# Kernel optimization log

Measured on AMD Instinct MI355X. Metric: run time of the kernel, lower is better.

The kernel has to match this reference:

```python
import jax, jax.numpy as jnp
import numpy as np

N_NODES = 100000
N_EDGES = 1600000
N_FEAT = 100
HIDDEN = 64
N_CLASSES = 47


def setup_inputs() -> dict:
    key = jax.random.key(0)
    k1, k2, k3, k4 = jax.random.split(key, 4)
    x = jax.random.normal(k1, (N_NODES, N_FEAT), dtype=jnp.float32)
    edge_index = jax.random.randint(k2, (2, N_EDGES), 0, N_NODES, dtype=jnp.int64)
    # Glorot-style init for GCNConv weights; zero bias (PyG default)
    W0 = jax.random.normal(k3, (N_FEAT, HIDDEN), dtype=jnp.float32) * (1.0 / np.sqrt(N_FEAT))
    b0 = jnp.zeros((HIDDEN,), dtype=jnp.float32)
    W1 = jax.random.normal(k4, (HIDDEN, N_CLASSES), dtype=jnp.float32) * (1.0 / np.sqrt(HIDDEN))
    b1 = jnp.zeros((N_CLASSES,), dtype=jnp.float32)
    return {"x": x, "edge_index": edge_index, "W0": W0, "b0": b0, "W1": W1, "b1": b1}


def _gcn_norm(edge_index, n_nodes):
    # PyG gcn_norm with add_self_loops=True, edge_weight=1
    loop = jnp.arange(n_nodes, dtype=edge_index.dtype)
    row = jnp.concatenate([edge_index[0], loop])  # source nodes
    col = jnp.concatenate([edge_index[1], loop])  # destination nodes
    ones = jnp.ones(row.shape[0], dtype=jnp.float32)
    deg = jax.ops.segment_sum(ones, col, num_segments=n_nodes)
    dinv = jnp.where(deg > 0, jax.lax.rsqrt(deg), 0.0)
    norm = dinv[row] * dinv[col]  # [E + N]
    return row, col, norm


def _gcn_conv(x, W, b, row, col, norm, n_nodes):
    # GCNConv: transform, then gather-scale-scatter aggregate, then bias
    xw = x @ W                                   # [N, out]
    msg = norm[:, None] * xw[row]                # [E+N, out]
    out = jax.ops.segment_sum(msg, col, num_segments=n_nodes)
    return out + b


def reference(x, edge_index, W0, b0, W1, b1):
    n_nodes = x.shape[0]
    row, col, norm = _gcn_norm(edge_index, n_nodes)  # same graph -> same norm per layer (cached)
    h = _gcn_conv(x, W0, b0, row, col, norm, n_nodes)
    h = jax.nn.relu(h)  # dropout is identity in eval mode
    out = _gcn_conv(h, W1, b1, row, col, norm, n_nodes)
    return out
```

## Files before the change

kernel.cpp:

```cpp
#include <hip/hip_runtime.h>
#include <hip/hip_fp16.h>

#define N_NODES   100000
#define N_EDGES   1600000
#define N_FEAT    100
#define HIDDEN    64
#define N_CLASSES 47
#define ZPAD      48
#define NBIN      ((N_NODES + 255) / 256)
#define SBLK      256
#define CHUNK     (N_EDGES / SBLK)
#define NHIST     (NBIN * SBLK)
#define WT0_ELEMS (HIDDEN * 128)
#define WT1_ELEMS (ZPAD * 64)

typedef _Float16 f16x8 __attribute__((ext_vector_type(8)));
typedef float f32x4 __attribute__((ext_vector_type(4)));


__global__ __launch_bounds__(256) void k_gscan1(const int* __restrict__ in,
                                                int* __restrict__ out,
                                                int* __restrict__ sums, int n) {
    __shared__ int tmp[256];
    int i = blockIdx.x * 256 + threadIdx.x;
    int v = (i < n) ? in[i] : 0;
    tmp[threadIdx.x] = v;
    __syncthreads();
    for (int off = 1; off < 256; off <<= 1) {
        int t = (threadIdx.x >= off) ? tmp[threadIdx.x - off] : 0;
        __syncthreads();
        tmp[threadIdx.x] += t;
        __syncthreads();
    }
    if (i < n) out[i] = tmp[threadIdx.x] - v;
    if (threadIdx.x == 255) sums[blockIdx.x] = tmp[255];
}

__global__ __launch_bounds__(512) void k_gscan2(int* __restrict__ sums, int nb) {
    __shared__ int tmp[512];
    int i = threadIdx.x;
    int v = (i < nb) ? sums[i] : 0;
    tmp[i] = v;
    __syncthreads();
    for (int off = 1; off < 512; off <<= 1) {
        int t = (i >= off) ? tmp[i - off] : 0;
        __syncthreads();
        tmp[i] += t;
        __syncthreads();
    }
    if (i < nb) sums[i] = tmp[i] - v;
}


__global__ __launch_bounds__(256) void k_hist(const int* __restrict__ ecol,
                                              int* __restrict__ gh) {
    __shared__ int lh[NBIN];
    int b = blockIdx.x, t = threadIdx.x;
    for (int i = t; i < NBIN; i += 256) lh[i] = 0;
    __syncthreads();
    int e0 = b * CHUNK;
    for (int i = t; i < CHUNK; i += 256)
        atomicAdd(&lh[ecol[e0 + i] >> 8], 1);
    __syncthreads();
    for (int i = t; i < NBIN; i += 256) gh[i * SBLK + b] = lh[i];
}

__global__ __launch_bounds__(256) void k_radix_scatter(
    const int* __restrict__ erow, const int* __restrict__ ecol,
    const int* __restrict__ gpos, const int* __restrict__ hsums,
    int* __restrict__ pairs) {
    __shared__ int lc[NBIN];
    int b = blockIdx.x, t = threadIdx.x;
    for (int i = t; i < NBIN; i += 256) lc[i] = gpos[i * SBLK + b] + hsums[i];
    __syncthreads();
    int e0 = b * CHUNK;
    for (int i = t; i < CHUNK; i += 256) {
        int e = e0 + i;
        int r = erow[e], c = ecol[e];
        int pos = atomicAdd(&lc[c >> 8], 1);
        pairs[pos] = r | ((c & 255) << 17);
    }
}

__global__ __launch_bounds__(256) void k_binfinish(
    const int* __restrict__ gpos, const int* __restrict__ hsums,
    const int* __restrict__ pairs,
    int* __restrict__ rp, float* __restrict__ dinv, int* __restrict__ eidx) {
    __shared__ int cnt[256];
    __shared__ int tmp[256];
    int b = blockIdx.x, t = threadIdx.x;
    int n0 = b << 8;
    int beg = gpos[b * SBLK] + hsums[b];
    int end = (b + 1 < NBIN) ? gpos[(b + 1) * SBLK] + hsums[b + 1] : N_EDGES;

    cnt[t] = 0;
    __syncthreads();
    for (int i = beg + t; i < end; i += 256)
        atomicAdd(&cnt[(pairs[i] >> 17) & 255], 1);
    __syncthreads();
    int v = cnt[t];
    tmp[t] = v;
    __syncthreads();
    for (int off = 1; off < 256; off <<= 1) {
        int u = (t >= off) ? tmp[t - off] : 0;
        __syncthreads();
        tmp[t] += u;
        __syncthreads();
    }
    int rpv = beg + tmp[t] - v;
    int n = n0 + t;
    if (n < N_NODES) {
        rp[n] = rpv;
        dinv[n] = rsqrtf(1.0f + (float)v);
    }
    if (b == NBIN - 1 && t == 0) rp[N_NODES] = N_EDGES;
    cnt[t] = rpv;
    __syncthreads();
    for (int i = beg + t; i < end; i += 256) {
        int p = pairs[i];
        int pos = atomicAdd(&cnt[(p >> 17) & 255], 1);
        eidx[pos] = p & 0x1FFFF;
    }
}

__global__ __launch_bounds__(256) void k_wprep(const float* __restrict__ W0,
                                               const float* __restrict__ W1,
                                               __half* __restrict__ wt0,
                                               __half* __restrict__ wt1) {
    int i = blockIdx.x * 256 + threadIdx.x;
    if (i < WT0_ELEMS) {
        int n = i >> 7, k = i & 127;
        wt0[i] = __float2half((k < N_FEAT) ? W0[k * HIDDEN + n] : 0.0f);
    } else if (i < WT0_ELEMS + WT1_ELEMS) {
        int j = i - WT0_ELEMS;
        int n = j >> 6, k = j & 63;
        wt1[j] = __float2half((n < N_CLASSES) ? W1[k * N_CLASSES + n] : 0.0f);
    }
}

__global__ __launch_bounds__(256) void k_gemm1(
    const float* __restrict__ x, const __half* __restrict__ wt0,
    const float* __restrict__ dinv, __half* __restrict__ yh) {
    int w = threadIdx.x >> 6, l = threadIdx.x & 63;
    int g = l >> 4, c16 = l & 15;
    int row = blockIdx.x * 64 + w * 16 + c16;
    int rl = (row < N_NODES) ? row : (N_NODES - 1);
    const float* xr = x + (size_t)rl * N_FEAT;

    f16x8 a[4];
    #pragma unroll
    for (int s = 0; s < 4; ++s) {
        int k0 = 32 * s + 8 * g;
        float4 f0 = (k0 + 3 < N_FEAT) ? *(const float4*)(xr + k0)
                                      : make_float4(0.f, 0.f, 0.f, 0.f);
        float4 f1 = (k0 + 7 < N_FEAT) ? *(const float4*)(xr + k0 + 4)
                                      : make_float4(0.f, 0.f, 0.f, 0.f);
        a[s][0] = (_Float16)f0.x; a[s][1] = (_Float16)f0.y;
        a[s][2] = (_Float16)f0.z; a[s][3] = (_Float16)f0.w;
        a[s][4] = (_Float16)f1.x; a[s][5] = (_Float16)f1.y;
        a[s][6] = (_Float16)f1.z; a[s][7] = (_Float16)f1.w;
    }
    f32x4 acc0 = {0,0,0,0}, acc1 = {0,0,0,0}, acc2 = {0,0,0,0}, acc3 = {0,0,0,0};
    #pragma unroll
    for (int s = 0; s < 4; ++s) {
        int ko = 32 * s + 8 * g;
        f16x8 b0 = *(const f16x8*)(wt0 + (0 * 16 + c16) * 128 + ko);
        f16x8 b1 = *(const f16x8*)(wt0 + (1 * 16 + c16) * 128 + ko);
        f16x8 b2 = *(const f16x8*)(wt0 + (2 * 16 + c16) * 128 + ko);
        f16x8 b3 = *(const f16x8*)(wt0 + (3 * 16 + c16) * 128 + ko);
        acc0 = __builtin_amdgcn_mfma_f32_16x16x32_f16(a[s], b0, acc0, 0, 0, 0);
        acc1 = __builtin_amdgcn_mfma_f32_16x16x32_f16(a[s], b1, acc1, 0, 0, 0);
        acc2 = __builtin_amdgcn_mfma_f32_16x16x32_f16(a[s], b2, acc2, 0, 0, 0);
        acc3 = __builtin_amdgcn_mfma_f32_16x16x32_f16(a[s], b3, acc3, 0, 0, 0);
    }
    int orow = blockIdx.x * 64 + w * 16 + 4 * g;
    #pragma unroll
    for (int r = 0; r < 4; ++r) {
        if (orow + r < N_NODES) {
            float di = dinv[orow + r];
            size_t base = (size_t)(orow + r) * HIDDEN + c16;
            yh[base +  0] = __float2half(di * acc0[r]);
            yh[base + 16] = __float2half(di * acc1[r]);
            yh[base + 32] = __float2half(di * acc2[r]);
            yh[base + 48] = __float2half(di * acc3[r]);
        }
    }
}

__global__ __launch_bounds__(256) void k_agg0(
    const int* __restrict__ rp, const int* __restrict__ eidx,
    const float* __restrict__ dinv, const __half* __restrict__ yh,
    const float* __restrict__ b0, const __half* __restrict__ wt1,
    __half* __restrict__ zh) {
    __shared__ __half hs[16][64];
    int t = blockIdx.x * 256 + threadIdx.x;
    int n = t >> 5;
    int hl = threadIdx.x & 31;
    int nl = threadIdx.x >> 5;

    ((__half2*)hs)[256 + threadIdx.x] = __floats2half2_rn(0.f, 0.f);

    int beg = rp[n], end = rp[n + 1];
    int deg = end - beg;
    int se = (beg + hl < end) ? eidx[beg + hl] : 0;
    const __half2* yh2 = (const __half2*)yh;
    float2 fs = __half22float2(yh2[(size_t)n * 32 + hl]);
    float ax = fs.x, ay = fs.y;
    int m = deg < 32 ? deg : 32;
    int base = threadIdx.x & 32;

    {
        int s0 = __shfl(se, base + 0),  s1 = __shfl(se, base + 1);
        int s2 = __shfl(se, base + 2),  s3 = __shfl(se, base + 3);
        int s4 = __shfl(se, base + 4),  s5 = __shfl(se, base + 5);
        int s6 = __shfl(se, base + 6),  s7 = __shfl(se, base + 7);
        int s8 = __shfl(se, base + 8),  s9 = __shfl(se, base + 9);
        int sa = __shfl(se, base + 10), sb = __shfl(se, base + 11);
        int sc = __shfl(se, base + 12), sd = __shfl(se, base + 13);
        int sec = __shfl(se, base + 14), sf = __shfl(se, base + 15);
        float2 f0 = __half22float2(yh2[(size_t)s0 * 32 + hl]);
        float2 f1 = __half22float2(yh2[(size_t)s1 * 32 + hl]);
        float2 f2 = __half22float2(yh2[(size_t)s2 * 32 + hl]);
        float2 f3 = __half22float2(yh2[(size_t)s3 * 32 + hl]);
        float2 f4 = __half22float2(yh2[(size_t)s4 * 32 + hl]);
        float2 f5 = __half22float2(yh2[(size_t)s5 * 32 + hl]);
        float2 f6 = __half22float2(yh2[(size_t)s6 * 32 + hl]);
        float2 f7 = __half22float2(yh2[(size_t)s7 * 32 + hl]);
        float2 f8 = __half22float2(yh2[(size_t)s8 * 32 + hl]);
        float2 f9 = __half22float2(yh2[(size_t)s9 * 32 + hl]);
        float2 fa = __half22float2(yh2[(size_t)sa * 32 + hl]);
        float2 fb = __half22float2(yh2[(size_t)sb * 32 + hl]);
        float2 fc = __half22float2(yh2[(size_t)sc * 32 + hl]);
        float2 fd = __half22float2(yh2[(size_t)sd * 32 + hl]);
        float2 fe = __half22float2(yh2[(size_t)sec * 32 + hl]);
        float2 ff = __half22float2(yh2[(size_t)sf * 32 + hl]);
        ax += ((m > 0  ? f0.x : 0.f) + (m > 1  ? f1.x : 0.f)) +
              ((m > 2  ? f2.x : 0.f) + (m > 3  ? f3.x : 0.f)) +
              ((m > 4  ? f4.x : 0.f) + (m > 5  ? f5.x : 0.f)) +
              ((m > 6  ? f6.x : 0.f) + (m > 7  ? f7.x : 0.f)) +
              ((m > 8  ? f8.x : 0.f) + (m > 9  ? f9.x : 0.f)) +
              ((m > 10 ? fa.x : 0.f) + (m > 11 ? fb.x : 0.f)) +
              ((m > 12 ? fc.x : 0.f) + (m > 13 ? fd.x : 0.f)) +
              ((m > 14 ? fe.x : 0.f) + (m > 15 ? ff.x : 0.f));
        ay += ((m > 0  ? f0.y : 0.f) + (m > 1  ? f1.y : 0.f)) +
              ((m > 2  ? f2.y : 0.f) + (m > 3  ? f3.y : 0.f)) +
              ((m > 4  ? f4.y : 0.f) + (m > 5  ? f5.y : 0.f)) +
              ((m > 6  ? f6.y : 0.f) + (m > 7  ? f7.y : 0.f)) +
              ((m > 8  ? f8.y : 0.f) + (m > 9  ? f9.y : 0.f)) +
              ((m > 10 ? fa.y : 0.f) + (m > 11 ? fb.y : 0.f)) +
              ((m > 12 ? fc.y : 0.f) + (m > 13 ? fd.y : 0.f)) +
              ((m > 14 ? fe.y : 0.f) + (m > 15 ? ff.y : 0.f));
    }
    if (m > 16) {
        int s0 = __shfl(se, base + 16), s1 = __shfl(se, base + 17);
        int s2 = __shfl(se, base + 18), s3 = __shfl(se, base + 19);
        int s4 = __shfl(se, base + 20), s5 = __shfl(se, base + 21);
        int s6 = __shfl(se, base + 22), s7 = __shfl(se, base + 23);
        int s8 = __shfl(se, base + 24), s9 = __shfl(se, base + 25);
        int sa = __shfl(se, base + 26), sb = __shfl(se, base + 27);
        int sc = __shfl(se, base + 28), sd = __shfl(se, base + 29);
        int sec = __shfl(se, base + 30), sf = __shfl(se, base + 31);
        float2 f0 = __half22float2(yh2[(size_t)s0 * 32 + hl]);
        float2 f1 = __half22float2(yh2[(size_t)s1 * 32 + hl]);
        float2 f2 = __half22float2(yh2[(size_t)s2 * 32 + hl]);
        float2 f3 = __half22float2(yh2[(size_t)s3 * 32 + hl]);
        float2 f4 = __half22float2(yh2[(size_t)s4 * 32 + hl]);
        float2 f5 = __half22float2(yh2[(size_t)s5 * 32 + hl]);
        float2 f6 = __half22float2(yh2[(size_t)s6 * 32 + hl]);
        float2 f7 = __half22float2(yh2[(size_t)s7 * 32 + hl]);
        float2 f8 = __half22float2(yh2[(size_t)s8 * 32 + hl]);
        float2 f9 = __half22float2(yh2[(size_t)s9 * 32 + hl]);
        float2 fa = __half22float2(yh2[(size_t)sa * 32 + hl]);
        float2 fb = __half22float2(yh2[(size_t)sb * 32 + hl]);
        float2 fc = __half22float2(yh2[(size_t)sc * 32 + hl]);
        float2 fd = __half22float2(yh2[(size_t)sd * 32 + hl]);
        float2 fe = __half22float2(yh2[(size_t)sec * 32 + hl]);
        float2 ff = __half22float2(yh2[(size_t)sf * 32 + hl]);
        ax += ((m > 16 ? f0.x : 0.f) + (m > 17 ? f1.x : 0.f)) +
              ((m > 18 ? f2.x : 0.f) + (m > 19 ? f3.x : 0.f)) +
              ((m > 20 ? f4.x : 0.f) + (m > 21 ? f5.x : 0.f)) +
              ((m > 22 ? f6.x : 0.f) + (m > 23 ? f7.x : 0.f)) +
              ((m > 24 ? f8.x : 0.f) + (m > 25 ? f9.x : 0.f)) +
              ((m > 26 ? fa.x : 0.f) + (m > 27 ? fb.x : 0.f)) +
              ((m > 28 ? fc.x : 0.f) + (m > 29 ? fd.x : 0.f)) +
              ((m > 30 ? fe.x : 0.f) + (m > 31 ? ff.x : 0.f));
        ay += ((m > 16 ? f0.y : 0.f) + (m > 17 ? f1.y : 0.f)) +
              ((m > 18 ? f2.y : 0.f) + (m > 19 ? f3.y : 0.f)) +
              ((m > 20 ? f4.y : 0.f) + (m > 21 ? f5.y : 0.f)) +
              ((m > 22 ? f6.y : 0.f) + (m > 23 ? f7.y : 0.f)) +
              ((m > 24 ? f8.y : 0.f) + (m > 25 ? f9.y : 0.f)) +
              ((m > 26 ? fa.y : 0.f) + (m > 27 ? fb.y : 0.f)) +
              ((m > 28 ? fc.y : 0.f) + (m > 29 ? fd.y : 0.f)) +
              ((m > 30 ? fe.y : 0.f) + (m > 31 ? ff.y : 0.f));
    }
    if (deg > 32) {
        for (int e = beg + 32; e < end; ++e) {
            int s = eidx[e];
            float2 fv = __half22float2(yh2[(size_t)s * 32 + hl]);
            ax += fv.x; ay += fv.y;
        }
    }
    float di = dinv[n];
    float2 b2 = ((const float2*)b0)[hl];
    float o0 = fmaxf(di * ax + b2.x, 0.0f);
    float o1 = fmaxf(di * ay + b2.y, 0.0f);
    ((__half2*)hs)[nl * 32 + hl] = __floats2half2_rn(o0, o1);
    __syncthreads();

    if (threadIdx.x < 64) {
        int l = threadIdx.x;
        int g = l >> 4, c16 = l & 15;
        f16x8 a0 = *(const f16x8*)(&hs[c16][8 * g]);
        f16x8 a1 = *(const f16x8*)(&hs[c16][32 + 8 * g]);
        f32x4 acc0 = {0,0,0,0}, acc1 = {0,0,0,0}, acc2 = {0,0,0,0};
        #pragma unroll
        for (int s = 0; s < 2; ++s) {
            int ko = 32 * s + 8 * g;
            f16x8 b0f = *(const f16x8*)(wt1 + (0 * 16 + c16) * 64 + ko);
            f16x8 b1f = *(const f16x8*)(wt1 + (1 * 16 + c16) * 64 + ko);
            f16x8 b2f = *(const f16x8*)(wt1 + (2 * 16 + c16) * 64 + ko);
            f16x8 av = s ? a1 : a0;
            acc0 = __builtin_amdgcn_mfma_f32_16x16x32_f16(av, b0f, acc0, 0, 0, 0);
            acc1 = __builtin_amdgcn_mfma_f32_16x16x32_f16(av, b1f, acc1, 0, 0, 0);
            acc2 = __builtin_amdgcn_mfma_f32_16x16x32_f16(av, b2f, acc2, 0, 0, 0);
        }
        if (g < 2) {
            int nrow = blockIdx.x * 8 + 4 * g;
            #pragma unroll
            for (int r = 0; r < 4; ++r) {
                float dr = dinv[nrow + r];
                size_t bz = (size_t)(nrow + r) * ZPAD + c16;
                zh[bz +  0] = __float2half(dr * acc0[r]);
                zh[bz + 16] = __float2half(dr * acc1[r]);
                zh[bz + 32] = __float2half(dr * acc2[r]);
            }
        }
    }
}

__global__ __launch_bounds__(256) void k_agg1(
    const int* __restrict__ rp, const int* __restrict__ eidx,
    const float* __restrict__ dinv, const __half* __restrict__ zh,
    const float* __restrict__ b1, float* __restrict__ out) {
    int t = blockIdx.x * 256 + threadIdx.x;
    int n = t >> 5;
    int hl = threadIdx.x & 31;
    if (n >= N_NODES) return;
    int beg = rp[n], end = rp[n + 1];
    int deg = end - beg;
    int se = (beg + hl < end) ? eidx[beg + hl] : 0;
    const __half2* zh2 = (const __half2*)zh;
    float ax = 0.0f, ay = 0.0f;
    if (hl < 24) {
        float2 f = __half22float2(zh2[(size_t)n * 24 + hl]);
        ax = f.x; ay = f.y;
    }
    int m = deg < 32 ? deg : 32;
    int base = threadIdx.x & 32;

    {
        int s0 = __shfl(se, base + 0),  s1 = __shfl(se, base + 1);
        int s2 = __shfl(se, base + 2),  s3 = __shfl(se, base + 3);
        int s4 = __shfl(se, base + 4),  s5 = __shfl(se, base + 5);
        int s6 = __shfl(se, base + 6),  s7 = __shfl(se, base + 7);
        int s8 = __shfl(se, base + 8),  s9 = __shfl(se, base + 9);
        int sa = __shfl(se, base + 10), sb = __shfl(se, base + 11);
        int sc = __shfl(se, base + 12), sd = __shfl(se, base + 13);
        int sec = __shfl(se, base + 14), sf = __shfl(se, base + 15);
        if (hl < 24) {
            float2 f0 = __half22float2(zh2[(size_t)s0 * 24 + hl]);
            float2 f1 = __half22float2(zh2[(size_t)s1 * 24 + hl]);
            float2 f2 = __half22float2(zh2[(size_t)s2 * 24 + hl]);
            float2 f3 = __half22float2(zh2[(size_t)s3 * 24 + hl]);
            float2 f4 = __half22float2(zh2[(size_t)s4 * 24 + hl]);
            float2 f5 = __half22float2(zh2[(size_t)s5 * 24 + hl]);
            float2 f6 = __half22float2(zh2[(size_t)s6 * 24 + hl]);
            float2 f7 = __half22float2(zh2[(size_t)s7 * 24 + hl]);
            float2 f8 = __half22float2(zh2[(size_t)s8 * 24 + hl]);
            float2 f9 = __half22float2(zh2[(size_t)s9 * 24 + hl]);
            float2 fa = __half22float2(zh2[(size_t)sa * 24 + hl]);
            float2 fb = __half22float2(zh2[(size_t)sb * 24 + hl]);
            float2 fc = __half22float2(zh2[(size_t)sc * 24 + hl]);
            float2 fd = __half22float2(zh2[(size_t)sd * 24 + hl]);
            float2 fe = __half22float2(zh2[(size_t)sec * 24 + hl]);
            float2 ff = __half22float2(zh2[(size_t)sf * 24 + hl]);
            ax += ((m > 0  ? f0.x : 0.f) + (m > 1  ? f1.x : 0.f)) +
                  ((m > 2  ? f2.x : 0.f) + (m > 3  ? f3.x : 0.f)) +
                  ((m > 4  ? f4.x : 0.f) + (m > 5  ? f5.x : 0.f)) +
                  ((m > 6  ? f6.x : 0.f) + (m > 7  ? f7.x : 0.f)) +
                  ((m > 8  ? f8.x : 0.f) + (m > 9  ? f9.x : 0.f)) +
                  ((m > 10 ? fa.x : 0.f) + (m > 11 ? fb.x : 0.f)) +
                  ((m > 12 ? fc.x : 0.f) + (m > 13 ? fd.x : 0.f)) +
                  ((m > 14 ? fe.x : 0.f) + (m > 15 ? ff.x : 0.f));
            ay += ((m > 0  ? f0.y : 0.f) + (m > 1  ? f1.y : 0.f)) +
                  ((m > 2  ? f2.y : 0.f) + (m > 3  ? f3.y : 0.f)) +
                  ((m > 4  ? f4.y : 0.f) + (m > 5  ? f5.y : 0.f)) +
                  ((m > 6  ? f6.y : 0.f) + (m > 7  ? f7.y : 0.f)) +
                  ((m > 8  ? f8.y : 0.f) + (m > 9  ? f9.y : 0.f)) +
                  ((m > 10 ? fa.y : 0.f) + (m > 11 ? fb.y : 0.f)) +
                  ((m > 12 ? fc.y : 0.f) + (m > 13 ? fd.y : 0.f)) +
                  ((m > 14 ? fe.y : 0.f) + (m > 15 ? ff.y : 0.f));
        }
    }
    if (m > 16) {
        int s0 = __shfl(se, base + 16), s1 = __shfl(se, base + 17);
        int s2 = __shfl(se, base + 18), s3 = __shfl(se, base + 19);
        int s4 = __shfl(se, base + 20), s5 = __shfl(se, base + 21);
        int s6 = __shfl(se, base + 22), s7 = __shfl(se, base + 23);
        int s8 = __shfl(se, base + 24), s9 = __shfl(se, base + 25);
        int sa = __shfl(se, base + 26), sb = __shfl(se, base + 27);
        int sc = __shfl(se, base + 28), sd = __shfl(se, base + 29);
        int sec = __shfl(se, base + 30), sf = __shfl(se, base + 31);
        if (hl < 24) {
            float2 f0 = __half22float2(zh2[(size_t)s0 * 24 + hl]);
            float2 f1 = __half22float2(zh2[(size_t)s1 * 24 + hl]);
            float2 f2 = __half22float2(zh2[(size_t)s2 * 24 + hl]);
            float2 f3 = __half22float2(zh2[(size_t)s3 * 24 + hl]);
            float2 f4 = __half22float2(zh2[(size_t)s4 * 24 + hl]);
            float2 f5 = __half22float2(zh2[(size_t)s5 * 24 + hl]);
            float2 f6 = __half22float2(zh2[(size_t)s6 * 24 + hl]);
            float2 f7 = __half22float2(zh2[(size_t)s7 * 24 + hl]);
            float2 f8 = __half22float2(zh2[(size_t)s8 * 24 + hl]);
            float2 f9 = __half22float2(zh2[(size_t)s9 * 24 + hl]);
            float2 fa = __half22float2(zh2[(size_t)sa * 24 + hl]);
            float2 fb = __half22float2(zh2[(size_t)sb * 24 + hl]);
            float2 fc = __half22float2(zh2[(size_t)sc * 24 + hl]);
            float2 fd = __half22float2(zh2[(size_t)sd * 24 + hl]);
            float2 fe = __half22float2(zh2[(size_t)sec * 24 + hl]);
            float2 ff = __half22float2(zh2[(size_t)sf * 24 + hl]);
            ax += ((m > 16 ? f0.x : 0.f) + (m > 17 ? f1.x : 0.f)) +
                  ((m > 18 ? f2.x : 0.f) + (m > 19 ? f3.x : 0.f)) +
                  ((m > 20 ? f4.x : 0.f) + (m > 21 ? f5.x : 0.f)) +
                  ((m > 22 ? f6.x : 0.f) + (m > 23 ? f7.x : 0.f)) +
                  ((m > 24 ? f8.x : 0.f) + (m > 25 ? f9.x : 0.f)) +
                  ((m > 26 ? fa.x : 0.f) + (m > 27 ? fb.x : 0.f)) +
                  ((m > 28 ? fc.x : 0.f) + (m > 29 ? fd.x : 0.f)) +
                  ((m > 30 ? fe.x : 0.f) + (m > 31 ? ff.x : 0.f));
            ay += ((m > 16 ? f0.y : 0.f) + (m > 17 ? f1.y : 0.f)) +
                  ((m > 18 ? f2.y : 0.f) + (m > 19 ? f3.y : 0.f)) +
                  ((m > 20 ? f4.y : 0.f) + (m > 21 ? f5.y : 0.f)) +
                  ((m > 22 ? f6.y : 0.f) + (m > 23 ? f7.y : 0.f)) +
                  ((m > 24 ? f8.y : 0.f) + (m > 25 ? f9.y : 0.f)) +
                  ((m > 26 ? fa.y : 0.f) + (m > 27 ? fb.y : 0.f)) +
                  ((m > 28 ? fc.y : 0.f) + (m > 29 ? fd.y : 0.f)) +
                  ((m > 30 ? fe.y : 0.f) + (m > 31 ? ff.y : 0.f));
        }
    }
    if (deg > 32) {
        for (int e = beg + 32; e < end; ++e) {
            int s = eidx[e];
            if (hl < 24) {
                float2 fv = __half22float2(zh2[(size_t)s * 24 + hl]);
                ax += fv.x; ay += fv.y;
            }
        }
    }
    if (hl < 24) {
        float di = dinv[n];
        out[(size_t)n * N_CLASSES + 2 * hl] = di * ax + b1[2 * hl];
        if (hl < 23)
            out[(size_t)n * N_CLASSES + 2 * hl + 1] = di * ay + b1[2 * hl + 1];
    }
}

extern "C" void kernel_launch(void* const* d_in, const int* in_sizes, int n_in,
                              void* d_out, int out_size, void* d_ws, size_t ws_size,
                              hipStream_t stream) {
    const float* x  = (const float*)d_in[0];
    const int*   ei = (const int*)d_in[1];
    const float* W0 = (const float*)d_in[2];
    const float* b0 = (const float*)d_in[3];
    const float* W1 = (const float*)d_in[4];
    const float* b1 = (const float*)d_in[5];
    float* out = (float*)d_out;

    char* ws = (char*)d_ws;
    float*  dinv  = (float*)(ws);
    int*    rp    = (int*)(ws + 412 * 1024);
    int*    hsums = (int*)(ws + 824 * 1024);
    int*    gh    = (int*)(ws + 828 * 1024);
    int*    gpos  = (int*)(ws + 1232 * 1024);
    __half* wt0   = (__half*)(ws + 1640 * 1024);
    __half* wt1   = (__half*)(ws + 1660 * 1024);
    int*    eidx  = (int*)(ws + 1668 * 1024);
    __half* yh    = (__half*)(ws + 9ull * 1024 * 1024);
    __half* zh    = (__half*)(ws + 22ull * 1024 * 1024);
    int*    pairs = (int*)zh;

    const int* erow = ei;
    const int* ecol = ei + N_EDGES;

    k_hist  <<<SBLK, 256, 0, stream>>>(ecol, gh);
    k_gscan1<<<NBIN, 256, 0, stream>>>(gh, gpos, hsums, NHIST);
    k_gscan2<<<1, 512, 0, stream>>>(hsums, NBIN);
    k_radix_scatter<<<SBLK, 256, 0, stream>>>(erow, ecol, gpos, hsums, pairs);
    k_binfinish<<<NBIN, 256, 0, stream>>>(gpos, hsums, pairs, rp, dinv, eidx);

    k_wprep<<<(WT0_ELEMS + WT1_ELEMS + 255) / 256, 256, 0, stream>>>(W0, W1, wt0, wt1);

    k_gemm1<<<(N_NODES + 63) / 64, 256, 0, stream>>>(x, wt0, dinv, yh);
    k_agg0 <<<(N_NODES * 32) / 256, 256, 0, stream>>>(rp, eidx, dinv, yh, b0, wt1, zh);

    k_agg1 <<<(N_NODES * 32) / 256, 256, 0, stream>>>(rp, eidx, dinv, zh, b1, out);
}
```

Measured before the change: 137.1 us.

## Fold weight prep into histogram kernel, double sort blocks, widen bin-finish blocks

Removes the separate weight-conversion kernel launch by doing the fp16 weight transpose inside the histogram kernel, whose 512 blocks cover all weight elements. The radix-sort partition count rises from 256 to 512, so each block handles a smaller edge chunk and the scan kernels use 512-thread blocks to match. The bin-finish kernel moves to 1024 threads per block so the counting and placement loops over each bin run with more parallelism. In exchange the global histogram and scan grow larger, and the workspace offsets are shifted to fit them.

```diff
diff --git a/kernel.cpp b/kernel.cpp
--- a/kernel.cpp
+++ b/kernel.cpp
@@ -8,32 +8,33 @@
 #define N_CLASSES 47
 #define ZPAD      48
 #define NBIN      ((N_NODES + 255) / 256)
-#define SBLK      256
+#define SBLK      512
 #define CHUNK     (N_EDGES / SBLK)
 #define NHIST     (NBIN * SBLK)
 #define WT0_ELEMS (HIDDEN * 128)
 #define WT1_ELEMS (ZPAD * 64)
+#define WPREP_N   (WT0_ELEMS + WT1_ELEMS)
 
 typedef _Float16 f16x8 __attribute__((ext_vector_type(8)));
 typedef float f32x4 __attribute__((ext_vector_type(4)));
 
 
-__global__ __launch_bounds__(256) void k_gscan1(const int* __restrict__ in,
+__global__ __launch_bounds__(512) void k_gscan1(const int* __restrict__ in,
                                                 int* __restrict__ out,
                                                 int* __restrict__ sums, int n) {
-    __shared__ int tmp[256];
-    int i = blockIdx.x * 256 + threadIdx.x;
+    __shared__ int tmp[512];
+    int i = blockIdx.x * 512 + threadIdx.x;
     int v = (i < n) ? in[i] : 0;
     tmp[threadIdx.x] = v;
     __syncthreads();
-    for (int off = 1; off < 256; off <<= 1) {
+    for (int off = 1; off < 512; off <<= 1) {
         int t = (threadIdx.x >= off) ? tmp[threadIdx.x - off] : 0;
         __syncthreads();
         tmp[threadIdx.x] += t;
         __syncthreads();
     }
     if (i < n) out[i] = tmp[threadIdx.x] - v;
-    if (threadIdx.x == 255) sums[blockIdx.x] = tmp[255];
+    if (threadIdx.x == 511) sums[blockIdx.x] = tmp[511];
 }
 
 __global__ __launch_bounds__(512) void k_gscan2(int* __restrict__ sums, int nb) {
@@ -53,7 +54,21 @@
 
 
 __global__ __launch_bounds__(256) void k_hist(const int* __restrict__ ecol,
-                                              int* __restrict__ gh) {
+                                              int* __restrict__ gh,
+                                              const float* __restrict__ W0,
+                                              const float* __restrict__ W1,
+                                              __half* __restrict__ wt0,
+                                              __half* __restrict__ wt1) {
+    int wi = blockIdx.x * 256 + threadIdx.x;
+    if (wi < WT0_ELEMS) {
+        int n = wi >> 7, k = wi & 127;
+        wt0[wi] = __float2half((k < N_FEAT) ? W0[k * HIDDEN + n] : 0.0f);
+    } else if (wi < WPREP_N) {
+        int j = wi - WT0_ELEMS;
+        int n = j >> 6, k = j & 63;
+        wt1[j] = __float2half((n < N_CLASSES) ? W1[k * N_CLASSES + n] : 0.0f);
+    }
+
     __shared__ int lh[NBIN];
     int b = blockIdx.x, t = threadIdx.x;
     for (int i = t; i < NBIN; i += 256) lh[i] = 0;
@@ -82,7 +97,7 @@
     }
 }
 
-__global__ __launch_bounds__(256) void k_binfinish(
+__global__ __launch_bounds__(1024) void k_binfinish(
     const int* __restrict__ gpos, const int* __restrict__ hsums,
     const int* __restrict__ pairs,
     int* __restrict__ rp, float* __restrict__ dinv, int* __restrict__ eidx) {
@@ -93,48 +108,35 @@
     int beg = gpos[b * SBLK] + hsums[b];
     int end = (b + 1 < NBIN) ? gpos[(b + 1) * SBLK] + hsums[b + 1] : N_EDGES;
 
-    cnt[t] = 0;
-    __syncthreads();
-    for (int i = beg + t; i < end; i += 256)
+    if (t < 256) cnt[t] = 0;
+    __syncthreads();
+    for (int i = beg + t; i < end; i += 1024)
         atomicAdd(&cnt[(pairs[i] >> 17) & 255], 1);
     __syncthreads();
-    int v = cnt[t];
-    tmp[t] = v;
+    int v = 0;
+    if (t < 256) { v = cnt[t]; tmp[t] = v; }
     __syncthreads();
     for (int off = 1; off < 256; off <<= 1) {
-        int u = (t >= off) ? tmp[t - off] : 0;
+        int u = (t < 256 && t >= off) ? tmp[t - off] : 0;
         __syncthreads();
-        tmp[t] += u;
+        if (t < 256) tmp[t] += u;
         __syncthreads();
     }
-    int rpv = beg + tmp[t] - v;
-    int n = n0 + t;
-    if (n < N_NODES) {
-        rp[n] = rpv;
-        dinv[n] = rsqrtf(1.0f + (float)v);
+    if (t < 256) {
+        int rpv = beg + tmp[t] - v;
+        int n = n0 + t;
+        if (n < N_NODES) {
+            rp[n] = rpv;
+            dinv[n] = rsqrtf(1.0f + (float)v);
+        }
+        cnt[t] = rpv;
     }
     if (b == NBIN - 1 && t == 0) rp[N_NODES] = N_EDGES;
-    cnt[t] = rpv;
-    __syncthreads();
-    for (int i = beg + t; i < end; i += 256) {
+    __syncthreads();
+    for (int i = beg + t; i < end; i += 1024) {
         int p = pairs[i];
         int pos = atomicAdd(&cnt[(p >> 17) & 255], 1);
         eidx[pos] = p & 0x1FFFF;
-    }
-}
-
-__global__ __launch_bounds__(256) void k_wprep(const float* __restrict__ W0,
-                                               const float* __restrict__ W1,
-                                               __half* __restrict__ wt0,
-                                               __half* __restrict__ wt1) {
-    int i = blockIdx.x * 256 + threadIdx.x;
-    if (i < WT0_ELEMS) {
-        int n = i >> 7, k = i & 127;
-        wt0[i] = __float2half((k < N_FEAT) ? W0[k * HIDDEN + n] : 0.0f);
-    } else if (i < WT0_ELEMS + WT1_ELEMS) {
-        int j = i - WT0_ELEMS;
-        int n = j >> 6, k = j & 63;
-        wt1[j] = __float2half((n < N_CLASSES) ? W1[k * N_CLASSES + n] : 0.0f);
     }
 }
 
@@ -479,24 +481,22 @@
     int*    rp    = (int*)(ws + 412 * 1024);
     int*    hsums = (int*)(ws + 824 * 1024);
     int*    gh    = (int*)(ws + 828 * 1024);
-    int*    gpos  = (int*)(ws + 1232 * 1024);
-    __half* wt0   = (__half*)(ws + 1640 * 1024);
-    __half* wt1   = (__half*)(ws + 1660 * 1024);
-    int*    eidx  = (int*)(ws + 1668 * 1024);
-    __half* yh    = (__half*)(ws + 9ull * 1024 * 1024);
-    __half* zh    = (__half*)(ws + 22ull * 1024 * 1024);
+    int*    gpos  = (int*)(ws + 1612 * 1024);
+    __half* wt0   = (__half*)(ws + 2400 * 1024);
+    __half* wt1   = (__half*)(ws + 2420 * 1024);
+    int*    eidx  = (int*)(ws + 2428 * 1024);
+    __half* yh    = (__half*)(ws + 10ull * 1024 * 1024);
+    __half* zh    = (__half*)(ws + 23ull * 1024 * 1024);
     int*    pairs = (int*)zh;
 
     const int* erow = ei;
     const int* ecol = ei + N_EDGES;
 
-    k_hist  <<<SBLK, 256, 0, stream>>>(ecol, gh);
-    k_gscan1<<<NBIN, 256, 0, stream>>>(gh, gpos, hsums, NHIST);
+    k_hist  <<<SBLK, 256, 0, stream>>>(ecol, gh, W0, W1, wt0, wt1);
+    k_gscan1<<<NBIN, 512, 0, stream>>>(gh, gpos, hsums, NHIST);
     k_gscan2<<<1, 512, 0, stream>>>(hsums, NBIN);
     k_radix_scatter<<<SBLK, 256, 0, stream>>>(erow, ecol, gpos, hsums, pairs);
-    k_binfinish<<<NBIN, 256, 0, stream>>>(gpos, hsums, pairs, rp, dinv, eidx);
-
-    k_wprep<<<(WT0_ELEMS + WT1_ELEMS + 255) / 256, 256, 0, stream>>>(W0, W1, wt0, wt1);
+    k_binfinish<<<NBIN, 1024, 0, stream>>>(gpos, hsums, pairs, rp, dinv, eidx);
 
     k_gemm1<<<(N_NODES + 63) / 64, 256, 0, stream>>>(x, wt0, dinv, yh);
     k_agg0 <<<(N_NODES * 32) / 256, 256, 0, stream>>>(rp, eidx, dinv, yh, b0, wt1, zh);
```

Result: faster. 133.5 us (-2.6%).
